# Optimization experiments

Hardware: AMD Instinct MI355X
Metric: run time of the kernel (lower is better)

The kernel has to match this reference:

```python
import jax, jax.numpy as jnp
import numpy as np

N_NODES = 100000
N_EDGES = 1600000
F_IN, F_HID, F_OUT = 256, 128, 32


def setup_inputs() -> dict:
    key = jax.random.key(0)
    k1, k2, k3, k4 = jax.random.split(key, 4)
    x = jax.random.normal(k1, (N_NODES, F_IN), dtype=jnp.float32)
    edge_index = jax.random.randint(k2, (2, N_EDGES), 0, N_NODES, dtype=jnp.int64)
    W1 = jax.random.normal(k3, (F_IN, F_HID), dtype=jnp.float32) * (1.0 / np.sqrt(F_IN))
    b1 = jnp.zeros((F_HID,), dtype=jnp.float32)
    W2 = jax.random.normal(k4, (F_HID, F_OUT), dtype=jnp.float32) * (1.0 / np.sqrt(F_HID))
    b2 = jnp.zeros((F_OUT,), dtype=jnp.float32)
    return {"x": x, "edge_index": edge_index, "W1": W1, "b1": b1, "W2": W2, "b2": b2}


def _gcn_norm(edge_index, num_nodes):
    # Add self-loops, then symmetric normalization deg^-1/2[src] * deg^-1/2[dst].
    loops = jnp.arange(num_nodes, dtype=edge_index.dtype)
    src = jnp.concatenate([edge_index[0], loops])
    dst = jnp.concatenate([edge_index[1], loops])
    deg = jax.ops.segment_sum(jnp.ones_like(dst, dtype=jnp.float32), dst,
                              num_segments=num_nodes)
    dinv = jnp.where(deg > 0, jax.lax.rsqrt(deg), 0.0)
    norm = dinv[src] * dinv[dst]  # [E + N]
    return src, dst, norm


def _gcn_conv(h, src, dst, norm, num_nodes):
    # h already linearly transformed. Gather sources, scale, scatter-add to dst.
    msgs = h[src] * norm[:, None]
    return jax.ops.segment_sum(msgs, dst, num_segments=num_nodes)


def reference(x, edge_index, W1, b1, W2, b2):
    n = x.shape[0]
    src, dst, norm = _gcn_norm(edge_index, n)
    # Layer 1: linear -> normalized scatter-add -> bias -> relu
    h = _gcn_conv(x @ W1, src, dst, norm, n) + b1
    h = jax.nn.relu(h)
    # F.dropout with training=False (eval mode) is identity.
    # Layer 2
    out = _gcn_conv(h @ W2, src, dst, norm, n) + b2
    return jax.nn.log_softmax(out, axis=1)
```

## Files before the change

### kernel.cpp

```cpp
#include <hip/hip_runtime.h>

#define N_NODES 100000
#define N_EDGES 1600000
#define F_IN 256
#define F_HID 128
#define F_OUT 32
#define NBUCK 391
#define BIN_BLOCKS 512
#define EDGES_PER_BIN 3125

typedef unsigned short ushort_t;
typedef unsigned int uint_t;

using short8  = __attribute__((ext_vector_type(8))) short;
using floatx4 = __attribute__((ext_vector_type(4))) float;

__device__ __forceinline__ ushort_t f2bf(float f) {
    uint_t u = __float_as_uint(f);
    u += 0x7fff + ((u >> 16) & 1);
    return (ushort_t)(u >> 16);
}
__device__ __forceinline__ float bf_lo(uint_t u) { return __uint_as_float(u << 16); }
__device__ __forceinline__ float bf_hi(uint_t u) { return __uint_as_float(u & 0xffff0000u); }
__device__ __forceinline__ uint_t bfpack_trunc(float a, float b) {
    return __builtin_amdgcn_perm(__float_as_uint(b), __float_as_uint(a), 0x07060302u);
}

__global__ __launch_bounds__(256) void histwt_kernel(const int* __restrict__ ei,
                                                     int* __restrict__ bucket_cnt,
                                                     const float* __restrict__ W1,
                                                     const float* __restrict__ W2,
                                                     ushort_t* __restrict__ W1T,
                                                     ushort_t* __restrict__ W2T) {
    __shared__ int h[NBUCK];
    if (blockIdx.x < BIN_BLOCKS) {
        for (int i = threadIdx.x; i < NBUCK; i += 256) h[i] = 0;
        __syncthreads();
        int gid = blockIdx.x * 256 + threadIdx.x;
        for (int e = gid; e < N_EDGES; e += BIN_BLOCKS * 256)
            atomicAdd(&h[ei[N_EDGES + e] >> 8], 1);
        __syncthreads();
        for (int i = threadIdx.x; i < NBUCK; i += 256) {
            int c = h[i];
            if (c) atomicAdd(&bucket_cnt[i], c);
        }
    } else {
        int t = (blockIdx.x - BIN_BLOCKS) * 256 + threadIdx.x;
#pragma unroll
        for (int j = 0; j < 4; j++) {
            int e = j * 8192 + t;
            int n = e >> 8, k = e & 255;
            W1T[e] = f2bf(W1[k * F_HID + n]);
        }
        if (t < 4096) {
            int n = t >> 7, k = t & 127;
            W2T[t] = f2bf(W2[k * F_OUT + n]);
        }
    }
}

__global__ __launch_bounds__(512) void scan_kernel(const int* __restrict__ bucket_cnt,
                                                   int* __restrict__ bucket_base,
                                                   int* __restrict__ bucket_cursor,
                                                   int* __restrict__ offs) {
    __shared__ int s[512];
    int t = threadIdx.x;
    int own = (t < NBUCK) ? bucket_cnt[t] : 0;
    s[t] = own;
    __syncthreads();
    for (int off = 1; off < 512; off <<= 1) {
        int v = (t >= off) ? s[t - off] : 0;
        __syncthreads();
        s[t] += v;
        __syncthreads();
    }
    if (t < NBUCK) {
        int ex = s[t] - own;
        bucket_base[t] = ex;
        bucket_cursor[t] = ex;
    }
    if (t == 0) {
        bucket_base[NBUCK] = N_EDGES;
        offs[N_NODES] = N_EDGES;
    }
}

__global__ __launch_bounds__(256) void bin_kernel(const int* __restrict__ ei,
                                                  int* __restrict__ bucket_cursor,
                                                  int2* __restrict__ binned) {
    __shared__ int h[NBUCK];
    __shared__ int base[NBUCK];
    const int t = threadIdx.x;
    const int beg = blockIdx.x * EDGES_PER_BIN;
    const int end = beg + EDGES_PER_BIN;
    for (int i = t; i < NBUCK; i += 256) h[i] = 0;
    __syncthreads();
    for (int e = beg + t; e < end; e += 256) atomicAdd(&h[ei[N_EDGES + e] >> 8], 1);
    __syncthreads();
    for (int i = t; i < NBUCK; i += 256) {
        int c = h[i];
        base[i] = c ? atomicAdd(&bucket_cursor[i], c) : 0;
        h[i] = 0;
    }
    __syncthreads();
    for (int e = beg + t; e < end; e += 256) {
        int s = ei[e], d = ei[N_EDGES + e];
        int bk = d >> 8;
        int p = base[bk] + atomicAdd(&h[bk], 1);
        binned[p] = make_int2(s, d);
    }
}

__global__ __launch_bounds__(256) void build_kernel(const int2* __restrict__ binned,
                                                    const int* __restrict__ bucket_base,
                                                    int* __restrict__ offs,
                                                    int* __restrict__ csr,
                                                    float* __restrict__ dinv) {
    __shared__ int h[256];
    __shared__ int sc[256];
    __shared__ int cur[256];
    const int b = blockIdx.x, t = threadIdx.x;
    const int beg = bucket_base[b];
    const int end = bucket_base[b + 1];
    h[t] = 0;
    __syncthreads();
    for (int j = beg + t; j < end; j += 256) {
        int2 p = binned[j];
        atomicAdd(&h[p.y & 255], 1);
    }
    __syncthreads();
    int deg = h[t];
    sc[t] = deg;
    __syncthreads();
    for (int off = 1; off < 256; off <<= 1) {
        int v = (t >= off) ? sc[t - off] : 0;
        __syncthreads();
        sc[t] += v;
        __syncthreads();
    }
    int excl = sc[t] - deg;
    cur[t] = excl;
    int node = b * 256 + t;
    if (node < N_NODES) {
        offs[node] = beg + excl;
        dinv[node] = rsqrtf((float)deg + 1.0f);
    }
    __syncthreads();
    for (int j = beg + t; j < end; j += 256) {
        int2 p = binned[j];
        int pos = atomicAdd(&cur[p.y & 255], 1);
        csr[beg + pos] = p.x;
    }
}

__global__ __launch_bounds__(512) void gemm1_kernel(const float* __restrict__ x,
                                                    const ushort_t* __restrict__ W1T,
                                                    ushort_t* __restrict__ h0bf) {
    __shared__ ushort_t Bst[F_HID][F_IN + 8];
    const int tid = threadIdx.x;
    const int rbase = blockIdx.x * 128;
    const int w = tid >> 6;
    const int lane = tid & 63;
    const int q = lane >> 4;
    const int nloc = lane & 15;

#pragma unroll
    for (int j = 0; j < 8; j++) {
        int f = j * 512 + tid;
        int n = f >> 5, kg = f & 31;
        uint4 v = ((const uint4*)(W1T + n * F_IN))[kg];
        *(uint4*)(&Bst[n][kg * 8]) = v;
    }
    __syncthreads();

    const int rowA = rbase + w * 16 + nloc;
    const bool okA = rowA < N_NODES;
    const float* ap = x + (size_t)rowA * F_IN + q * 8;

    floatx4 acc[8];
#pragma unroll
    for (int t = 0; t < 8; t++) acc[t] = (floatx4){0.f, 0.f, 0.f, 0.f};

#pragma unroll
    for (int k0 = 0; k0 < F_IN; k0 += 32) {
        float4 f0 = make_float4(0.f, 0.f, 0.f, 0.f);
        float4 f1 = make_float4(0.f, 0.f, 0.f, 0.f);
        if (okA) {
            f0 = *(const float4*)(ap + k0);
            f1 = *(const float4*)(ap + k0 + 4);
        }
        uint4 au;
        au.x = bfpack_trunc(f0.x, f0.y);
        au.y = bfpack_trunc(f0.z, f0.w);
        au.z = bfpack_trunc(f1.x, f1.y);
        au.w = bfpack_trunc(f1.z, f1.w);
        short8 a = *(short8*)&au;
#pragma unroll
        for (int t = 0; t < 8; t++) {
            short8 b = *(const short8*)(&Bst[t * 16 + nloc][k0 + q * 8]);
            acc[t] = __builtin_amdgcn_mfma_f32_16x16x32_bf16(a, b, acc[t], 0, 0, 0);
        }
    }

#pragma unroll
    for (int reg = 0; reg < 4; reg++) {
        int rowD = rbase + w * 16 + q * 4 + reg;
        if (rowD < N_NODES) {
            ushort_t* op = h0bf + (size_t)rowD * F_HID + nloc;
#pragma unroll
            for (int t = 0; t < 8; t++) op[t * 16] = f2bf(acc[t][reg]);
        }
    }
}

__global__ __launch_bounds__(256) void gather128(const ushort_t* __restrict__ h0bf,
                                                 const int* __restrict__ offs,
                                                 const int* __restrict__ csr,
                                                 const float* __restrict__ dinv,
                                                 ushort_t* __restrict__ aggbf) {
    int node = blockIdx.x * 8 + (threadIdx.x >> 5);
    int l = threadIdx.x & 31;
    float dn = dinv[node];
    uint2 sv = ((const uint2*)(h0bf + (size_t)node * F_HID))[l];
    float s = dn * dn;
    float4 acc;
    acc.x = bf_lo(sv.x) * s; acc.y = bf_hi(sv.x) * s;
    acc.z = bf_lo(sv.y) * s; acc.w = bf_hi(sv.y) * s;

    int beg = offs[node], end = offs[node + 1];
    int j = beg;
    for (; j + 3 < end; j += 4) {
        int s0 = csr[j], s1 = csr[j + 1], s2 = csr[j + 2], s3 = csr[j + 3];
        float n0 = dinv[s0] * dn, n1 = dinv[s1] * dn;
        float n2 = dinv[s2] * dn, n3 = dinv[s3] * dn;
        uint2 v0 = ((const uint2*)(h0bf + (size_t)s0 * F_HID))[l];
        uint2 v1 = ((const uint2*)(h0bf + (size_t)s1 * F_HID))[l];
        uint2 v2 = ((const uint2*)(h0bf + (size_t)s2 * F_HID))[l];
        uint2 v3 = ((const uint2*)(h0bf + (size_t)s3 * F_HID))[l];
        acc.x += bf_lo(v0.x) * n0 + bf_lo(v1.x) * n1 + bf_lo(v2.x) * n2 + bf_lo(v3.x) * n3;
        acc.y += bf_hi(v0.x) * n0 + bf_hi(v1.x) * n1 + bf_hi(v2.x) * n2 + bf_hi(v3.x) * n3;
        acc.z += bf_lo(v0.y) * n0 + bf_lo(v1.y) * n1 + bf_lo(v2.y) * n2 + bf_lo(v3.y) * n3;
        acc.w += bf_hi(v0.y) * n0 + bf_hi(v1.y) * n1 + bf_hi(v2.y) * n2 + bf_hi(v3.y) * n3;
    }
    for (; j < end; j++) {
        int s0 = csr[j];
        float n0 = dinv[s0] * dn;
        uint2 v0 = ((const uint2*)(h0bf + (size_t)s0 * F_HID))[l];
        acc.x += bf_lo(v0.x) * n0; acc.y += bf_hi(v0.x) * n0;
        acc.z += bf_lo(v0.y) * n0; acc.w += bf_hi(v0.y) * n0;
    }
    uint2 p;
    p.x = (uint_t)f2bf(acc.x) | ((uint_t)f2bf(acc.y) << 16);
    p.y = (uint_t)f2bf(acc.z) | ((uint_t)f2bf(acc.w) << 16);
    ((uint2*)(aggbf + (size_t)node * F_HID))[l] = p;
}

__global__ __launch_bounds__(256) void gemm2_kernel(const ushort_t* __restrict__ aggbf,
                                                    const float* __restrict__ b1,
                                                    const ushort_t* __restrict__ W2T,
                                                    ushort_t* __restrict__ h2bf) {
    __shared__ ushort_t Bs[F_OUT][F_HID + 8];
    __shared__ float b1s[F_HID];
    const int tid = threadIdx.x;
    const int rbase = blockIdx.x * 64;
    const int w = tid >> 6;
    const int lane = tid & 63;
    const int q = lane >> 4;
    const int nloc = lane & 15;

    if (tid < F_HID) b1s[tid] = b1[tid];
#pragma unroll
    for (int jj = 0; jj < 2; jj++) {
        int f = jj * 256 + tid;
        int n = f >> 4, kg = f & 15;
        uint4 v = ((const uint4*)(W2T + n * F_HID))[kg];
        *(uint4*)(&Bs[n][kg * 8]) = v;
    }
    __syncthreads();

    const int rowA = rbase + w * 16 + nloc;
    const bool okA = rowA < N_NODES;

    floatx4 acc[2];
    acc[0] = (floatx4){0.f, 0.f, 0.f, 0.f};
    acc[1] = (floatx4){0.f, 0.f, 0.f, 0.f};

#pragma unroll
    for (int k0 = 0; k0 < F_HID; k0 += 32) {
        int kk = k0 + q * 8;
        uint4 av = make_uint4(0, 0, 0, 0);
        if (okA) av = *(const uint4*)(aggbf + (size_t)rowA * F_HID + kk);
        float4 bb0 = *(const float4*)(&b1s[kk]);
        float4 bb1 = *(const float4*)(&b1s[kk + 4]);
        uint4 au;
        au.x = bfpack_trunc(fmaxf(bf_lo(av.x) + bb0.x, 0.f), fmaxf(bf_hi(av.x) + bb0.y, 0.f));
        au.y = bfpack_trunc(fmaxf(bf_lo(av.y) + bb0.z, 0.f), fmaxf(bf_hi(av.y) + bb0.w, 0.f));
        au.z = bfpack_trunc(fmaxf(bf_lo(av.z) + bb1.x, 0.f), fmaxf(bf_hi(av.z) + bb1.y, 0.f));
        au.w = bfpack_trunc(fmaxf(bf_lo(av.w) + bb1.z, 0.f), fmaxf(bf_hi(av.w) + bb1.w, 0.f));
        short8 a = *(short8*)&au;
#pragma unroll
        for (int t = 0; t < 2; t++) {
            short8 b = *(const short8*)(&Bs[t * 16 + nloc][kk]);
            acc[t] = __builtin_amdgcn_mfma_f32_16x16x32_bf16(a, b, acc[t], 0, 0, 0);
        }
    }
#pragma unroll
    for (int reg = 0; reg < 4; reg++) {
        int rowD = rbase + w * 16 + q * 4 + reg;
        if (rowD < N_NODES) {
            ushort_t* op = h2bf + (size_t)rowD * F_OUT + nloc;
            op[0]  = f2bf(acc[0][reg]);
            op[16] = f2bf(acc[1][reg]);
        }
    }
}

__global__ __launch_bounds__(256) void gather32_lsm(const ushort_t* __restrict__ h2bf,
                                                    const int* __restrict__ offs,
                                                    const int* __restrict__ csr,
                                                    const float* __restrict__ dinv,
                                                    const float* __restrict__ b2,
                                                    float* __restrict__ out) {
    int node = blockIdx.x * 32 + (threadIdx.x >> 3);
    int l = threadIdx.x & 7;
    float dn = dinv[node];
    uint2 sv = ((const uint2*)(h2bf + (size_t)node * F_OUT))[l];
    float s = dn * dn;
    float4 acc;
    acc.x = bf_lo(sv.x) * s; acc.y = bf_hi(sv.x) * s;
    acc.z = bf_lo(sv.y) * s; acc.w = bf_hi(sv.y) * s;

    int beg = offs[node], end = offs[node + 1];
    int j = beg;
    for (; j + 3 < end; j += 4) {
        int s0 = csr[j], s1 = csr[j + 1], s2 = csr[j + 2], s3 = csr[j + 3];
        float n0 = dinv[s0] * dn, n1 = dinv[s1] * dn;
        float n2 = dinv[s2] * dn, n3 = dinv[s3] * dn;
        uint2 v0 = ((const uint2*)(h2bf + (size_t)s0 * F_OUT))[l];
        uint2 v1 = ((const uint2*)(h2bf + (size_t)s1 * F_OUT))[l];
        uint2 v2 = ((const uint2*)(h2bf + (size_t)s2 * F_OUT))[l];
        uint2 v3 = ((const uint2*)(h2bf + (size_t)s3 * F_OUT))[l];
        acc.x += bf_lo(v0.x) * n0 + bf_lo(v1.x) * n1 + bf_lo(v2.x) * n2 + bf_lo(v3.x) * n3;
        acc.y += bf_hi(v0.x) * n0 + bf_hi(v1.x) * n1 + bf_hi(v2.x) * n2 + bf_hi(v3.x) * n3;
        acc.z += bf_lo(v0.y) * n0 + bf_lo(v1.y) * n1 + bf_lo(v2.y) * n2 + bf_lo(v3.y) * n3;
        acc.w += bf_hi(v0.y) * n0 + bf_hi(v1.y) * n1 + bf_hi(v2.y) * n2 + bf_hi(v3.y) * n3;
    }
    for (; j < end; j++) {
        int s0 = csr[j];
        float n0 = dinv[s0] * dn;
        uint2 v0 = ((const uint2*)(h2bf + (size_t)s0 * F_OUT))[l];
        acc.x += bf_lo(v0.x) * n0; acc.y += bf_hi(v0.x) * n0;
        acc.z += bf_lo(v0.y) * n0; acc.w += bf_hi(v0.y) * n0;
    }
    float4 bb = ((const float4*)b2)[l];
    acc.x += bb.x; acc.y += bb.y; acc.z += bb.z; acc.w += bb.w;

    float m = fmaxf(fmaxf(acc.x, acc.y), fmaxf(acc.z, acc.w));
#pragma unroll
    for (int off = 1; off < 8; off <<= 1) m = fmaxf(m, __shfl_xor(m, off, 8));
    float es = __expf(acc.x - m) + __expf(acc.y - m) + __expf(acc.z - m) + __expf(acc.w - m);
#pragma unroll
    for (int off = 1; off < 8; off <<= 1) es += __shfl_xor(es, off, 8);
    float lse = m + __logf(es);
    float4 o = make_float4(acc.x - lse, acc.y - lse, acc.z - lse, acc.w - lse);
    ((float4*)(out + (size_t)node * F_OUT))[l] = o;
}

extern "C" void kernel_launch(void* const* d_in, const int* in_sizes, int n_in,
                              void* d_out, int out_size, void* d_ws, size_t ws_size,
                              hipStream_t stream) {
    const float* x  = (const float*)d_in[0];
    const int*   ei = (const int*)d_in[1];
    const float* W1 = (const float*)d_in[2];
    const float* b1 = (const float*)d_in[3];
    const float* W2 = (const float*)d_in[4];
    const float* b2 = (const float*)d_in[5];
    float* out = (float*)d_out;

    float* ws = (float*)d_ws;
    float*    dinv          = ws;
    int*      offs          = (int*)(ws + 100096);
    int*      bucket_cnt    = (int*)(ws + 200224);
    int*      bucket_base   = (int*)(ws + 200736);
    int*      bucket_cursor = (int*)(ws + 201248);
    int*      csr           = (int*)(ws + 201760);
    ushort_t* W1T           = (ushort_t*)(ws + 1801760);
    ushort_t* W2T           = (ushort_t*)(ws + 1818144);
    ushort_t* h0bf          = (ushort_t*)(ws + 1820192);
    ushort_t* aggbf         = (ushort_t*)(ws + 8220192);
    ushort_t* h2bf          = (ushort_t*)(ws + 14620192);
    int2*     binned        = (int2*)aggbf;

    hipMemsetAsync(bucket_cnt, 0, 512 * sizeof(int), stream);
    histwt_kernel<<<BIN_BLOCKS + 32, 256, 0, stream>>>(ei, bucket_cnt, W1, W2, W1T, W2T);
    scan_kernel<<<1, 512, 0, stream>>>(bucket_cnt, bucket_base, bucket_cursor, offs);
    bin_kernel<<<BIN_BLOCKS, 256, 0, stream>>>(ei, bucket_cursor, binned);
    build_kernel<<<NBUCK, 256, 0, stream>>>(binned, bucket_base, offs, csr, dinv);
    gemm1_kernel<<<(N_NODES + 127) / 128, 512, 0, stream>>>(x, W1T, h0bf);
    gather128<<<N_NODES / 8, 256, 0, stream>>>(h0bf, offs, csr, dinv, aggbf);
    gemm2_kernel<<<(N_NODES + 63) / 64, 256, 0, stream>>>(aggbf, b1, W2T, h2bf);
    gather32_lsm<<<N_NODES / 32, 256, 0, stream>>>(h2bf, offs, csr, dinv, b2, out);
}
```

Measured before the change: 350.2 us.

## Pack source degree into CSR entries and widen gather loads with edge-parallel lanes

A new pack pass stores each source node's degree in the upper 12 bits of its CSR entry, so the gathers rebuild the normalisation with rsqrt instead of a dependent dinv[src] load. Both gather kernels are restructured so each wave splits edges across sub-groups that issue 16-byte row loads, with more loads in flight per iteration. Partial sums are combined by cross-lane shuffles at the end. The cost is an extra pass over the CSR, and the packing assumes node ids below 2^20 and degrees below 4096. The vectorised CSR reads may also run past the end of the array, though the results of those lanes are masked out.

```diff
diff --git a/kernel.cpp b/kernel.cpp
--- a/kernel.cpp
+++ b/kernel.cpp
@@ -115,7 +115,8 @@
                                                     const int* __restrict__ bucket_base,
                                                     int* __restrict__ offs,
                                                     int* __restrict__ csr,
-                                                    float* __restrict__ dinv) {
+                                                    float* __restrict__ dinv,
+                                                    int* __restrict__ degarr) {
     __shared__ int h[256];
     __shared__ int sc[256];
     __shared__ int cur[256];
@@ -144,6 +145,7 @@
     if (node < N_NODES) {
         offs[node] = beg + excl;
         dinv[node] = rsqrtf((float)deg + 1.0f);
+        degarr[node] = deg;
     }
     __syncthreads();
     for (int j = beg + t; j < end; j += 256) {
@@ -151,6 +153,18 @@
         int pos = atomicAdd(&cur[p.y & 255], 1);
         csr[beg + pos] = p.x;
     }
+}
+
+__global__ __launch_bounds__(256) void pack_kernel(int* __restrict__ csr,
+                                                   const int* __restrict__ degarr) {
+    int i = blockIdx.x * 256 + threadIdx.x;
+    if (i >= N_EDGES / 4) return;
+    int4 c = ((int4*)csr)[i];
+    c.x |= degarr[c.x] << 20;
+    c.y |= degarr[c.y] << 20;
+    c.z |= degarr[c.z] << 20;
+    c.w |= degarr[c.w] << 20;
+    ((int4*)csr)[i] = c;
 }
 
 __global__ __launch_bounds__(512) void gemm1_kernel(const float* __restrict__ x,
@@ -218,41 +232,54 @@
                                                  const int* __restrict__ csr,
                                                  const float* __restrict__ dinv,
                                                  ushort_t* __restrict__ aggbf) {
-    int node = blockIdx.x * 8 + (threadIdx.x >> 5);
-    int l = threadIdx.x & 31;
-    float dn = dinv[node];
-    uint2 sv = ((const uint2*)(h0bf + (size_t)node * F_HID))[l];
-    float s = dn * dn;
-    float4 acc;
-    acc.x = bf_lo(sv.x) * s; acc.y = bf_hi(sv.x) * s;
-    acc.z = bf_lo(sv.y) * s; acc.w = bf_hi(sv.y) * s;
-
-    int beg = offs[node], end = offs[node + 1];
-    int j = beg;
-    for (; j + 3 < end; j += 4) {
-        int s0 = csr[j], s1 = csr[j + 1], s2 = csr[j + 2], s3 = csr[j + 3];
-        float n0 = dinv[s0] * dn, n1 = dinv[s1] * dn;
-        float n2 = dinv[s2] * dn, n3 = dinv[s3] * dn;
-        uint2 v0 = ((const uint2*)(h0bf + (size_t)s0 * F_HID))[l];
-        uint2 v1 = ((const uint2*)(h0bf + (size_t)s1 * F_HID))[l];
-        uint2 v2 = ((const uint2*)(h0bf + (size_t)s2 * F_HID))[l];
-        uint2 v3 = ((const uint2*)(h0bf + (size_t)s3 * F_HID))[l];
-        acc.x += bf_lo(v0.x) * n0 + bf_lo(v1.x) * n1 + bf_lo(v2.x) * n2 + bf_lo(v3.x) * n3;
-        acc.y += bf_hi(v0.x) * n0 + bf_hi(v1.x) * n1 + bf_hi(v2.x) * n2 + bf_hi(v3.x) * n3;
-        acc.z += bf_lo(v0.y) * n0 + bf_lo(v1.y) * n1 + bf_lo(v2.y) * n2 + bf_lo(v3.y) * n3;
-        acc.w += bf_hi(v0.y) * n0 + bf_hi(v1.y) * n1 + bf_hi(v2.y) * n2 + bf_hi(v3.y) * n3;
-    }
-    for (; j < end; j++) {
-        int s0 = csr[j];
-        float n0 = dinv[s0] * dn;
-        uint2 v0 = ((const uint2*)(h0bf + (size_t)s0 * F_HID))[l];
-        acc.x += bf_lo(v0.x) * n0; acc.y += bf_hi(v0.x) * n0;
-        acc.z += bf_lo(v0.y) * n0; acc.w += bf_hi(v0.y) * n0;
-    }
-    uint2 p;
-    p.x = (uint_t)f2bf(acc.x) | ((uint_t)f2bf(acc.y) << 16);
-    p.y = (uint_t)f2bf(acc.z) | ((uint_t)f2bf(acc.w) << 16);
-    ((uint2*)(aggbf + (size_t)node * F_HID))[l] = p;
+    const int node = blockIdx.x * 8 + (threadIdx.x >> 5);
+    const int l = threadIdx.x & 31;
+    const int sub = l >> 4;
+    const int fl = l & 15;
+    const float dn = dinv[node];
+    const uint4* rowbase = (const uint4*)h0bf;
+
+    uint4 sv = rowbase[(size_t)node * 16 + fl];
+    float s = (sub == 0) ? dn * dn : 0.f;
+    float a[8];
+    a[0] = bf_lo(sv.x) * s; a[1] = bf_hi(sv.x) * s;
+    a[2] = bf_lo(sv.y) * s; a[3] = bf_hi(sv.y) * s;
+    a[4] = bf_lo(sv.z) * s; a[5] = bf_hi(sv.z) * s;
+    a[6] = bf_lo(sv.w) * s; a[7] = bf_hi(sv.w) * s;
+
+    const int beg = offs[node], end = offs[node + 1];
+    for (int j = beg; j < end; j += 16) {
+        uint_t w[8];
+        float nn[8];
+        uint4 r[8];
+#pragma unroll
+        for (int k = 0; k < 8; k++) w[k] = ((const uint_t*)csr)[j + 2 * k + sub];
+#pragma unroll
+        for (int k = 0; k < 8; k++) {
+            bool v = (j + 2 * k + sub) < end;
+            int src = v ? (int)(w[k] & 0xFFFFFu) : 0;
+            nn[k] = v ? rsqrtf((float)(w[k] >> 20) + 1.0f) * dn : 0.f;
+            r[k] = rowbase[(size_t)src * 16 + fl];
+        }
+#pragma unroll
+        for (int k = 0; k < 8; k++) {
+            float n = nn[k];
+            a[0] += bf_lo(r[k].x) * n; a[1] += bf_hi(r[k].x) * n;
+            a[2] += bf_lo(r[k].y) * n; a[3] += bf_hi(r[k].y) * n;
+            a[4] += bf_lo(r[k].z) * n; a[5] += bf_hi(r[k].z) * n;
+            a[6] += bf_lo(r[k].w) * n; a[7] += bf_hi(r[k].w) * n;
+        }
+    }
+#pragma unroll
+    for (int i = 0; i < 8; i++) a[i] += __shfl_xor(a[i], 16);
+    if (sub == 0) {
+        uint4 p;
+        p.x = (uint_t)f2bf(a[0]) | ((uint_t)f2bf(a[1]) << 16);
+        p.y = (uint_t)f2bf(a[2]) | ((uint_t)f2bf(a[3]) << 16);
+        p.z = (uint_t)f2bf(a[4]) | ((uint_t)f2bf(a[5]) << 16);
+        p.w = (uint_t)f2bf(a[6]) | ((uint_t)f2bf(a[7]) << 16);
+        ((uint4*)aggbf)[(size_t)node * 16 + fl] = p;
+    }
 }
 
 __global__ __launch_bounds__(256) void gemm2_kernel(const ushort_t* __restrict__ aggbf,
@@ -321,49 +348,74 @@
                                                     const float* __restrict__ dinv,
                                                     const float* __restrict__ b2,
                                                     float* __restrict__ out) {
-    int node = blockIdx.x * 32 + (threadIdx.x >> 3);
-    int l = threadIdx.x & 7;
-    float dn = dinv[node];
-    uint2 sv = ((const uint2*)(h2bf + (size_t)node * F_OUT))[l];
-    float s = dn * dn;
-    float4 acc;
-    acc.x = bf_lo(sv.x) * s; acc.y = bf_hi(sv.x) * s;
-    acc.z = bf_lo(sv.y) * s; acc.w = bf_hi(sv.y) * s;
-
-    int beg = offs[node], end = offs[node + 1];
-    int j = beg;
-    for (; j + 3 < end; j += 4) {
-        int s0 = csr[j], s1 = csr[j + 1], s2 = csr[j + 2], s3 = csr[j + 3];
-        float n0 = dinv[s0] * dn, n1 = dinv[s1] * dn;
-        float n2 = dinv[s2] * dn, n3 = dinv[s3] * dn;
-        uint2 v0 = ((const uint2*)(h2bf + (size_t)s0 * F_OUT))[l];
-        uint2 v1 = ((const uint2*)(h2bf + (size_t)s1 * F_OUT))[l];
-        uint2 v2 = ((const uint2*)(h2bf + (size_t)s2 * F_OUT))[l];
-        uint2 v3 = ((const uint2*)(h2bf + (size_t)s3 * F_OUT))[l];
-        acc.x += bf_lo(v0.x) * n0 + bf_lo(v1.x) * n1 + bf_lo(v2.x) * n2 + bf_lo(v3.x) * n3;
-        acc.y += bf_hi(v0.x) * n0 + bf_hi(v1.x) * n1 + bf_hi(v2.x) * n2 + bf_hi(v3.x) * n3;
-        acc.z += bf_lo(v0.y) * n0 + bf_lo(v1.y) * n1 + bf_lo(v2.y) * n2 + bf_lo(v3.y) * n3;
-        acc.w += bf_hi(v0.y) * n0 + bf_hi(v1.y) * n1 + bf_hi(v2.y) * n2 + bf_hi(v3.y) * n3;
-    }
-    for (; j < end; j++) {
-        int s0 = csr[j];
-        float n0 = dinv[s0] * dn;
-        uint2 v0 = ((const uint2*)(h2bf + (size_t)s0 * F_OUT))[l];
-        acc.x += bf_lo(v0.x) * n0; acc.y += bf_hi(v0.x) * n0;
-        acc.z += bf_lo(v0.y) * n0; acc.w += bf_hi(v0.y) * n0;
-    }
-    float4 bb = ((const float4*)b2)[l];
-    acc.x += bb.x; acc.y += bb.y; acc.z += bb.z; acc.w += bb.w;
-
-    float m = fmaxf(fmaxf(acc.x, acc.y), fmaxf(acc.z, acc.w));
-#pragma unroll
-    for (int off = 1; off < 8; off <<= 1) m = fmaxf(m, __shfl_xor(m, off, 8));
-    float es = __expf(acc.x - m) + __expf(acc.y - m) + __expf(acc.z - m) + __expf(acc.w - m);
-#pragma unroll
-    for (int off = 1; off < 8; off <<= 1) es += __shfl_xor(es, off, 8);
+    const int node = blockIdx.x * 8 + (threadIdx.x >> 5);
+    const int l = threadIdx.x & 31;
+    const int sub = l >> 2;
+    const int fl = l & 3;
+    const float dn = dinv[node];
+    const uint4* rowbase = (const uint4*)h2bf;
+
+    uint4 sv = rowbase[(size_t)node * 4 + fl];
+    float s = (sub == 0) ? dn * dn : 0.f;
+    float a[8];
+    a[0] = bf_lo(sv.x) * s; a[1] = bf_hi(sv.x) * s;
+    a[2] = bf_lo(sv.y) * s; a[3] = bf_hi(sv.y) * s;
+    a[4] = bf_lo(sv.z) * s; a[5] = bf_hi(sv.z) * s;
+    a[6] = bf_lo(sv.w) * s; a[7] = bf_hi(sv.w) * s;
+
+    const int beg = offs[node], end = offs[node + 1];
+    for (int j = beg; j < end; j += 16) {
+        uint_t w[2];
+        float nn[2];
+        uint4 r[2];
+#pragma unroll
+        for (int k = 0; k < 2; k++) w[k] = ((const uint_t*)csr)[j + 8 * k + sub];
+#pragma unroll
+        for (int k = 0; k < 2; k++) {
+            bool v = (j + 8 * k + sub) < end;
+            int src = v ? (int)(w[k] & 0xFFFFFu) : 0;
+            nn[k] = v ? rsqrtf((float)(w[k] >> 20) + 1.0f) * dn : 0.f;
+            r[k] = rowbase[(size_t)src * 4 + fl];
+        }
+#pragma unroll
+        for (int k = 0; k < 2; k++) {
+            float n = nn[k];
+            a[0] += bf_lo(r[k].x) * n; a[1] += bf_hi(r[k].x) * n;
+            a[2] += bf_lo(r[k].y) * n; a[3] += bf_hi(r[k].y) * n;
+            a[4] += bf_lo(r[k].z) * n; a[5] += bf_hi(r[k].z) * n;
+            a[6] += bf_lo(r[k].w) * n; a[7] += bf_hi(r[k].w) * n;
+        }
+    }
+#pragma unroll
+    for (int i = 0; i < 8; i++) {
+        a[i] += __shfl_xor(a[i], 4);
+        a[i] += __shfl_xor(a[i], 8);
+        a[i] += __shfl_xor(a[i], 16);
+    }
+    float4 bb0 = ((const float4*)b2)[fl * 2];
+    float4 bb1 = ((const float4*)b2)[fl * 2 + 1];
+    a[0] += bb0.x; a[1] += bb0.y; a[2] += bb0.z; a[3] += bb0.w;
+    a[4] += bb1.x; a[5] += bb1.y; a[6] += bb1.z; a[7] += bb1.w;
+
+    float m = a[0];
+#pragma unroll
+    for (int i = 1; i < 8; i++) m = fmaxf(m, a[i]);
+    m = fmaxf(m, __shfl_xor(m, 1));
+    m = fmaxf(m, __shfl_xor(m, 2));
+    float es = 0.f;
+#pragma unroll
+    for (int i = 0; i < 8; i++) es += __expf(a[i] - m);
+    es += __shfl_xor(es, 1);
+    es += __shfl_xor(es, 2);
     float lse = m + __logf(es);
-    float4 o = make_float4(acc.x - lse, acc.y - lse, acc.z - lse, acc.w - lse);
-    ((float4*)(out + (size_t)node * F_OUT))[l] = o;
+
+    if (sub == 0) {
+        float4 o0 = make_float4(a[0] - lse, a[1] - lse, a[2] - lse, a[3] - lse);
+        float4 o1 = make_float4(a[4] - lse, a[5] - lse, a[6] - lse, a[7] - lse);
+        float4* op = (float4*)(out + (size_t)node * F_OUT);
+        op[fl * 2] = o0;
+        op[fl * 2 + 1] = o1;
+    }
 }
 
 extern "C" void kernel_launch(void* const* d_in, const int* in_sizes, int n_in,
@@ -383,21 +435,23 @@
     int*      bucket_cnt    = (int*)(ws + 200224);
     int*      bucket_base   = (int*)(ws + 200736);
     int*      bucket_cursor = (int*)(ws + 201248);
-    int*      csr           = (int*)(ws + 201760);
-    ushort_t* W1T           = (ushort_t*)(ws + 1801760);
-    ushort_t* W2T           = (ushort_t*)(ws + 1818144);
-    ushort_t* h0bf          = (ushort_t*)(ws + 1820192);
-    ushort_t* aggbf         = (ushort_t*)(ws + 8220192);
-    ushort_t* h2bf          = (ushort_t*)(ws + 14620192);
+    int*      degarr        = (int*)(ws + 201760);
+    int*      csr           = (int*)(ws + 301856);
+    ushort_t* W1T           = (ushort_t*)(ws + 1901856);
+    ushort_t* W2T           = (ushort_t*)(ws + 1918240);
+    ushort_t* h0bf          = (ushort_t*)(ws + 1920288);
+    ushort_t* aggbf         = (ushort_t*)(ws + 8320288);
+    ushort_t* h2bf          = (ushort_t*)(ws + 14720288);
     int2*     binned        = (int2*)aggbf;
 
     hipMemsetAsync(bucket_cnt, 0, 512 * sizeof(int), stream);
     histwt_kernel<<<BIN_BLOCKS + 32, 256, 0, stream>>>(ei, bucket_cnt, W1, W2, W1T, W2T);
     scan_kernel<<<1, 512, 0, stream>>>(bucket_cnt, bucket_base, bucket_cursor, offs);
     bin_kernel<<<BIN_BLOCKS, 256, 0, stream>>>(ei, bucket_cursor, binned);
-    build_kernel<<<NBUCK, 256, 0, stream>>>(binned, bucket_base, offs, csr, dinv);
+    build_kernel<<<NBUCK, 256, 0, stream>>>(binned, bucket_base, offs, csr, dinv, degarr);
+    pack_kernel<<<(N_EDGES / 4 + 255) / 256, 256, 0, stream>>>(csr, degarr);
     gemm1_kernel<<<(N_NODES + 127) / 128, 512, 0, stream>>>(x, W1T, h0bf);
     gather128<<<N_NODES / 8, 256, 0, stream>>>(h0bf, offs, csr, dinv, aggbf);
     gemm2_kernel<<<(N_NODES + 63) / 64, 256, 0, stream>>>(aggbf, b1, W2T, h2bf);
-    gather32_lsm<<<N_NODES / 32, 256, 0, stream>>>(h2bf, offs, csr, dinv, b2, out);
-}
+    gather32_lsm<<<N_NODES / 8, 256, 0, stream>>>(h2bf, offs, csr, dinv, b2, out);
+}
```

Result: no change. 349.5 us (-0.2%).
